# Kernel optimization log

Measured on AMD Instinct MI355X. Metric: run time of the kernel, lower is better.

Reference implementation:

```python
import jax, jax.numpy as jnp
import numpy as np

B = 16384      # batch
D_IN = 512     # layer_channels[0]
D = 1024       # hidden width (layer_channels[1..4])
R = 16         # num_relations
SCALE = 0.02


def setup_inputs() -> dict:
    key = jax.random.key(0)
    ks = jax.random.split(key, 8)
    return {
        "x": jax.random.normal(ks[0], (B, D_IN), dtype=jnp.float32),
        "relations": jax.random.randint(ks[1], (B,), 0, R, dtype=jnp.int32),
        # non-relation dense stack (2 layers)
        "W0": jax.random.normal(ks[2], (D_IN, D), dtype=jnp.float32) * SCALE,
        "b0": jnp.zeros((D,), dtype=jnp.float32),
        "W1": jax.random.normal(ks[3], (D, D), dtype=jnp.float32) * SCALE,
        "b1": jnp.zeros((D,), dtype=jnp.float32),
        # relation-aware layers (3 layers due to the module's range(i, num_layers))
        "RW1": jax.random.normal(ks[4], (R, D, D), dtype=jnp.float32) * SCALE,
        "Rb1": jnp.zeros((R, D), dtype=jnp.float32),
        "RW2": jax.random.normal(ks[5], (R, D, D), dtype=jnp.float32) * SCALE,
        "Rb2": jnp.zeros((R, D), dtype=jnp.float32),
        "RW3": jax.random.normal(ks[6], (R, D, D), dtype=jnp.float32) * SCALE,
        "Rb3": jnp.zeros((R, D), dtype=jnp.float32),
    }


def _relation_linear(h, W, b, relations):
    """Per-sample weight selection: out[n] = h[n] @ W[rel[n]] + b[rel[n]].
    Computed as R masked GEMMs to avoid materializing per-sample [B,D,D] weights.
    """
    out = jnp.zeros((h.shape[0], W.shape[2]), dtype=h.dtype)
    for r in range(W.shape[0]):  # fixed small expert set -> ok to unroll
        mask = (relations == r)[:, None]
        out = out + jnp.where(mask, h @ W[r] + b[r], jnp.zeros((), h.dtype))
    return out


def reference(x, relations, W0, b0, W1, b1, RW1, Rb1, RW2, Rb2, RW3, Rb3):
    # non_relation_pred: Linear -> ReLU -> (dropout=identity), twice
    h = jax.nn.relu(x @ W0 + b0)
    h = jax.nn.relu(h @ W1 + b1)
    # relation layers: relu+dropout between, none after last; bn disabled
    h = jax.nn.relu(_relation_linear(h, RW1, Rb1, relations))
    h = jax.nn.relu(_relation_linear(h, RW2, Rb2, relations))
    h = _relation_linear(h, RW3, Rb3, relations)
    return h
```

## Files before the change

### kernel.cpp

```cpp
#include <hip/hip_runtime.h>
#include <stdint.h>

#define B_ROWS   16384
#define D_IN     512
#define N_DIM    1024
#define NREL     16
#define TM       128
#define TN       128
#define BK       32
#define MAX_TILES 144
#define PADDED_ROWS (MAX_TILES * TM)

typedef __bf16 bf16x8 __attribute__((ext_vector_type(8)));
typedef float  f32x4  __attribute__((ext_vector_type(4)));

__device__ __forceinline__ uint16_t f2bf(float f) {
  union { float f; uint32_t u; } v; v.f = f;
  return (uint16_t)((v.u + 0x7fffu + ((v.u >> 16) & 1u)) >> 16);
}

__device__ __forceinline__ void async_cp16(const uint16_t* g, uint16_t* l) {
  __builtin_amdgcn_global_load_lds(
      (__attribute__((address_space(1))) void*)(g),
      (__attribute__((address_space(3))) void*)(l), 16, 0, 0);
}

__global__ void setup_kernel(const int* __restrict__ rel, int* __restrict__ rowidx,
                             int* __restrict__ texp, int* __restrict__ tval) {
  __shared__ int cnt[NREL], segstart[NREL], cursor[NREL];
  const int t = threadIdx.x;
  const int nt_ = blockDim.x;
  if (t < NREL) { cnt[t] = 0; cursor[t] = 0; }
  __syncthreads();
  for (int i = t; i < B_ROWS; i += nt_) atomicAdd(&cnt[rel[i]], 1);
  __syncthreads();
  if (t == 0) {
    int slot = 0, tile = 0;
    for (int r = 0; r < NREL; r++) {
      segstart[r] = slot;
      const int c = cnt[r];
      const int nt = (c + TM - 1) / TM;
      for (int k = 0; k < nt; k++) {
        texp[tile + k] = r;
        const int rem = c - k * TM;
        tval[tile + k] = rem < TM ? rem : TM;
      }
      tile += nt; slot += nt * TM;
    }
    for (; tile < MAX_TILES; tile++) { texp[tile] = 0; tval[tile] = 0; }
  }
  __syncthreads();
  for (int i = t; i < PADDED_ROWS; i += nt_) rowidx[i] = 0;
  __syncthreads();
  for (int i = t; i < B_ROWS; i += nt_) {
    const int r = rel[i];
    const int p = atomicAdd(&cursor[r], 1);
    rowidx[segstart[r] + p] = i;
  }
}

__global__ void conv_x_kernel(const float* __restrict__ in, uint16_t* __restrict__ out, int n4) {
  const int i = blockIdx.x * blockDim.x + threadIdx.x;
  if (i < n4) {
    const float4 v = ((const float4*)in)[i];
    uint2 o;
    o.x = (uint32_t)f2bf(v.x) | ((uint32_t)f2bf(v.y) << 16);
    o.y = (uint32_t)f2bf(v.z) | ((uint32_t)f2bf(v.w) << 16);
    ((uint2*)out)[i] = o;
  }
}

__global__ __launch_bounds__(256)
void transpose_conv_kernel(const float* __restrict__ W, uint16_t* __restrict__ Wt,
                           int K, int N) {
  __shared__ uint32_t t32[64][33];
  const size_t mat = (size_t)K * N;
  const float*    Wp  = W  + mat * blockIdx.z;
  uint16_t*       Wtp = Wt + mat * blockIdx.z;
  const int n0 = blockIdx.x * 64, k0 = blockIdx.y * 64;
  const int tx = threadIdx.x & 15;
  const int ty = threadIdx.x >> 4;
  #pragma unroll
  for (int rb = 0; rb < 2; rb++) {
    const int kp = rb * 16 + ty;
    const int k  = k0 + kp * 2;
    const float4 r0 = *(const float4*)&Wp[(size_t)k * N + n0 + tx * 4];
    const float4 r1 = *(const float4*)&Wp[(size_t)(k + 1) * N + n0 + tx * 4];
    t32[tx * 4 + 0][kp] = (uint32_t)f2bf(r0.x) | ((uint32_t)f2bf(r1.x) << 16);
    t32[tx * 4 + 1][kp] = (uint32_t)f2bf(r0.y) | ((uint32_t)f2bf(r1.y) << 16);
    t32[tx * 4 + 2][kp] = (uint32_t)f2bf(r0.z) | ((uint32_t)f2bf(r1.z) << 16);
    t32[tx * 4 + 3][kp] = (uint32_t)f2bf(r0.w) | ((uint32_t)f2bf(r1.w) << 16);
  }
  __syncthreads();
  #pragma unroll
  for (int rb = 0; rb < 4; rb++) {
    const int nl = rb * 16 + ty;
    uint2 v; v.x = t32[nl][2 * tx]; v.y = t32[nl][2 * tx + 1];
    *(uint2*)&Wtp[(size_t)(n0 + nl) * K + k0 + tx * 4] = v;
  }
}

template<bool GATHER, bool EXPERT, bool RELU, bool SCATTER>
__global__ __launch_bounds__(256)
void gemm_kernel(const uint16_t* __restrict__ A, const uint16_t* __restrict__ W,
                 const float* __restrict__ bias, void* __restrict__ outp,
                 const int* __restrict__ rowidx, const int* __restrict__ texp,
                 const int* __restrict__ tval, int K) {
  __shared__ uint16_t sA[2][TM * BK];
  __shared__ uint16_t sB[2][TN * BK];

  const int tid = threadIdx.x;
  const int w = tid >> 6, l = tid & 63;

  const int lin = blockIdx.x;
  const int xcd = lin & 7;
  const int j   = lin >> 3;
  const int mpx = gridDim.x >> 6;
  const int my  = xcd * mpx + (j >> 3);
  const int nx  = j & 7;
  const int m0 = my * TM;
  const int n0 = nx * TN;

  int e = 0, valid = TM;
  if (EXPERT) {
    e = texp[my];
    valid = tval[my];
    if (valid == 0) return;
  }

  const int row0   = 16 * w + (l >> 2);
  const int sel    = (row0 ^ (row0 >> 2)) & 3;
  const int koff   = ((l & 3) ^ sel) * 8;
  int ar0 = m0 + row0, ar1 = m0 + 64 + row0;
  if (GATHER) { ar0 = rowidx[ar0]; ar1 = rowidx[ar1]; }
  const uint16_t* srcA0 = A + (size_t)ar0 * K + koff;
  const uint16_t* srcA1 = A + (size_t)ar1 * K + koff;
  const uint16_t* Wb    = W + (size_t)e * N_DIM * K;
  const uint16_t* srcB0 = Wb + (size_t)(n0 + row0) * K + koff;
  const uint16_t* srcB1 = Wb + (size_t)(n0 + 64 + row0) * K + koff;
  uint16_t* ldsA0 = &sA[0][w * 512 + l * 8];
  uint16_t* ldsA1 = &sA[0][2048 + w * 512 + l * 8];
  uint16_t* ldsB0 = &sB[0][w * 512 + l * 8];
  uint16_t* ldsB1 = &sB[0][2048 + w * 512 + l * 8];

  const int wm = w >> 1, wn = w & 1;
  const int q = l >> 4, r16 = l & 15;
  const int selr = (r16 ^ (r16 >> 2)) & 3;
  const int cq = (q ^ selr) * 8;

  f32x4 acc[4][4];
  #pragma unroll
  for (int i = 0; i < 4; i++)
    #pragma unroll
    for (int jj = 0; jj < 4; jj++) {
      f32x4 z = {0.f, 0.f, 0.f, 0.f};
      acc[i][jj] = z;
    }

  const int nIter = K / BK;

  async_cp16(srcA0, ldsA0);
  async_cp16(srcA1, ldsA1);
  async_cp16(srcB0, ldsB0);
  async_cp16(srcB1, ldsB1);

  for (int k = 0; k < nIter; k++) {
    const int cur = k & 1;
    if (k + 1 < nIter) {
      const int koff2 = (k + 1) * BK;
      const int boff  = (cur ^ 1) * 4096;
      async_cp16(srcA0 + koff2, ldsA0 + boff);
      async_cp16(srcA1 + koff2, ldsA1 + boff);
      async_cp16(srcB0 + koff2, ldsB0 + boff);
      async_cp16(srcB1 + koff2, ldsB1 + boff);
      asm volatile("s_waitcnt vmcnt(4)" ::: "memory");
    } else {
      asm volatile("s_waitcnt vmcnt(0)" ::: "memory");
    }
    __builtin_amdgcn_s_barrier();

    bf16x8 af[4], bf[4];
    #pragma unroll
    for (int i = 0; i < 4; i++) {
      af[i] = *(const bf16x8*)(&sA[cur][(wm * 64 + i * 16 + r16) * BK + cq]);
      bf[i] = *(const bf16x8*)(&sB[cur][(wn * 64 + i * 16 + r16) * BK + cq]);
    }
    #pragma unroll
    for (int i = 0; i < 4; i++)
      #pragma unroll
      for (int jj = 0; jj < 4; jj++)
        acc[i][jj] = __builtin_amdgcn_mfma_f32_16x16x32_bf16(af[i], bf[jj], acc[i][jj], 0, 0, 0);

    __builtin_amdgcn_s_barrier();
  }

  float bj[4];
  #pragma unroll
  for (int jj = 0; jj < 4; jj++)
    bj[jj] = bias[(size_t)e * N_DIM + n0 + wn * 64 + jj * 16 + r16];

  #pragma unroll
  for (int i = 0; i < 4; i++) {
    #pragma unroll
    for (int r = 0; r < 4; r++) {
      const int rl = wm * 64 + i * 16 + q * 4 + r;
      if (SCATTER) {
        if (rl < valid) {
          const int orow = rowidx[m0 + rl];
          float* o = (float*)outp + (size_t)orow * N_DIM + n0 + wn * 64 + r16;
          #pragma unroll
          for (int jj = 0; jj < 4; jj++) {
            float v = acc[i][jj][r] + bj[jj];
            if (RELU) v = fmaxf(v, 0.f);
            o[jj * 16] = v;
          }
        }
      } else {
        uint16_t* o = (uint16_t*)outp + (size_t)(m0 + rl) * N_DIM + n0 + wn * 64 + r16;
        #pragma unroll
        for (int jj = 0; jj < 4; jj++) {
          float v = acc[i][jj][r] + bj[jj];
          if (RELU) v = fmaxf(v, 0.f);
          o[jj * 16] = f2bf(v);
        }
      }
    }
  }
}

extern "C" void kernel_launch(void* const* d_in, const int* in_sizes, int n_in,
                              void* d_out, int out_size, void* d_ws, size_t ws_size,
                              hipStream_t stream) {
  const float* x   = (const float*)d_in[0];
  const int*   rel = (const int*)d_in[1];
  const float* W0  = (const float*)d_in[2];
  const float* b0  = (const float*)d_in[3];
  const float* W1  = (const float*)d_in[4];
  const float* b1  = (const float*)d_in[5];
  const float* RW1 = (const float*)d_in[6];
  const float* Rb1 = (const float*)d_in[7];
  const float* RW2 = (const float*)d_in[8];
  const float* Rb2 = (const float*)d_in[9];
  const float* RW3 = (const float*)d_in[10];
  const float* Rb3 = (const float*)d_in[11];
  float* out = (float*)d_out;

  char* ws = (char*)d_ws;
  uint16_t* xb = (uint16_t*)(ws);
  uint16_t* wt = (uint16_t*)(ws + (size_t)(16u << 20));
  uint16_t* ha = (uint16_t*)(ws + (size_t)(48u << 20));
  uint16_t* hb = (uint16_t*)(ws + (size_t)(84u << 20));
  int* rowidx = (int*)(ws + (size_t)(120u << 20));
  int* texp   = rowidx + PADDED_ROWS;
  int* tval   = texp + MAX_TILES;

  const dim3 blk(256);
  const dim3 gDense(8 * (B_ROWS / TM));
  const dim3 gRel(8 * MAX_TILES);

  setup_kernel<<<dim3(1), dim3(1024), 0, stream>>>(rel, rowidx, texp, tval);
  conv_x_kernel<<<dim3((B_ROWS * D_IN) / 4 / 256), blk, 0, stream>>>(x, xb, (B_ROWS * D_IN) / 4);

  transpose_conv_kernel<<<dim3(N_DIM / 64, D_IN / 64, 1), blk, 0, stream>>>(W0, wt, D_IN, N_DIM);
  gemm_kernel<false, false, true, false><<<gDense, blk, 0, stream>>>(
      xb, wt, b0, ha, nullptr, nullptr, nullptr, D_IN);

  transpose_conv_kernel<<<dim3(N_DIM / 64, N_DIM / 64, 1), blk, 0, stream>>>(W1, wt, N_DIM, N_DIM);
  gemm_kernel<false, false, true, false><<<gDense, blk, 0, stream>>>(
      ha, wt, b1, hb, nullptr, nullptr, nullptr, N_DIM);

  transpose_conv_kernel<<<dim3(N_DIM / 64, N_DIM / 64, NREL), blk, 0, stream>>>(RW1, wt, N_DIM, N_DIM);
  gemm_kernel<true, true, true, false><<<gRel, blk, 0, stream>>>(
      hb, wt, Rb1, ha, rowidx, texp, tval, N_DIM);

  transpose_conv_kernel<<<dim3(N_DIM / 64, N_DIM / 64, NREL), blk, 0, stream>>>(RW2, wt, N_DIM, N_DIM);
  gemm_kernel<false, true, true, false><<<gRel, blk, 0, stream>>>(
      ha, wt, Rb2, hb, rowidx, texp, tval, N_DIM);

  transpose_conv_kernel<<<dim3(N_DIM / 64, N_DIM / 64, NREL), blk, 0, stream>>>(RW3, wt, N_DIM, N_DIM);
  gemm_kernel<false, true, false, true><<<gRel, blk, 0, stream>>>(
      hb, wt, Rb3, out, rowidx, texp, tval, N_DIM);

  (void)in_sizes; (void)n_in; (void)out_size; (void)ws_size;
}
```

Baseline: 517.5 us.

## Deepen GEMM LDS pipeline to four stages with fragment prefetch and setprio

Replaces the double-buffered async global-to-LDS loop with a four-stage ring buffer. Four K-slices are kept in flight, and the LDS fragments for the next slice are read into registers while the current MFMAs run. The loop now uses a single barrier per iteration instead of two, and it raises wave priority around the MFMA block. The aim is to hide global-load latency and LDS read latency behind matrix math. In exchange, LDS per block doubles to 64KB, which may lower the number of resident blocks per CU.

```diff
diff --git a/kernel.cpp b/kernel.cpp
--- a/kernel.cpp
+++ b/kernel.cpp
@@ -106,8 +106,8 @@
                  const float* __restrict__ bias, void* __restrict__ outp,
                  const int* __restrict__ rowidx, const int* __restrict__ texp,
                  const int* __restrict__ tval, int K) {
-  __shared__ uint16_t sA[2][TM * BK];
-  __shared__ uint16_t sB[2][TN * BK];
+  __shared__ uint16_t sA[4][TM * BK];
+  __shared__ uint16_t sB[4][TN * BK];
 
   const int tid = threadIdx.x;
   const int w = tid >> 6, l = tid & 63;
@@ -138,10 +138,7 @@
   const uint16_t* Wb    = W + (size_t)e * N_DIM * K;
   const uint16_t* srcB0 = Wb + (size_t)(n0 + row0) * K + koff;
   const uint16_t* srcB1 = Wb + (size_t)(n0 + 64 + row0) * K + koff;
-  uint16_t* ldsA0 = &sA[0][w * 512 + l * 8];
-  uint16_t* ldsA1 = &sA[0][2048 + w * 512 + l * 8];
-  uint16_t* ldsB0 = &sB[0][w * 512 + l * 8];
-  uint16_t* ldsB1 = &sB[0][2048 + w * 512 + l * 8];
+  const int lo = w * 512 + l * 8;
 
   const int wm = w >> 1, wn = w & 1;
   const int q = l >> 4, r16 = l & 15;
@@ -157,42 +154,69 @@
       acc[i][jj] = z;
     }
 
-  const int nIter = K / BK;
-
-  async_cp16(srcA0, ldsA0);
-  async_cp16(srcA1, ldsA1);
-  async_cp16(srcB0, ldsB0);
-  async_cp16(srcB1, ldsB1);
-
-  for (int k = 0; k < nIter; k++) {
-    const int cur = k & 1;
-    if (k + 1 < nIter) {
-      const int koff2 = (k + 1) * BK;
-      const int boff  = (cur ^ 1) * 4096;
-      async_cp16(srcA0 + koff2, ldsA0 + boff);
-      async_cp16(srcA1 + koff2, ldsA1 + boff);
-      async_cp16(srcB0 + koff2, ldsB0 + boff);
-      async_cp16(srcB1 + koff2, ldsB1 + boff);
-      asm volatile("s_waitcnt vmcnt(4)" ::: "memory");
-    } else {
-      asm volatile("s_waitcnt vmcnt(0)" ::: "memory");
-    }
-    __builtin_amdgcn_s_barrier();
-
-    bf16x8 af[4], bf[4];
+  bf16x8 af[4], bf[4];
+
+  auto STAGE = [&](int h) {
+    const int s  = h & 3;
+    const int ko = h * BK;
+    async_cp16(srcA0 + ko, &sA[s][lo]);
+    async_cp16(srcA1 + ko, &sA[s][2048 + lo]);
+    async_cp16(srcB0 + ko, &sB[s][lo]);
+    async_cp16(srcB1 + ko, &sB[s][2048 + lo]);
+  };
+  auto READF = [&](int h) {
+    const int s = h & 3;
     #pragma unroll
     for (int i = 0; i < 4; i++) {
-      af[i] = *(const bf16x8*)(&sA[cur][(wm * 64 + i * 16 + r16) * BK + cq]);
-      bf[i] = *(const bf16x8*)(&sB[cur][(wn * 64 + i * 16 + r16) * BK + cq]);
+      af[i] = *(const bf16x8*)(&sA[s][(wm * 64 + i * 16 + r16) * BK + cq]);
+      bf[i] = *(const bf16x8*)(&sB[s][(wn * 64 + i * 16 + r16) * BK + cq]);
     }
+  };
+  auto MFMAS = [&]() {
     #pragma unroll
     for (int i = 0; i < 4; i++)
       #pragma unroll
       for (int jj = 0; jj < 4; jj++)
         acc[i][jj] = __builtin_amdgcn_mfma_f32_16x16x32_bf16(af[i], bf[jj], acc[i][jj], 0, 0, 0);
-
+  };
+
+  const int NPH = K / BK;
+
+  STAGE(0); STAGE(1); STAGE(2); STAGE(3);
+  asm volatile("s_waitcnt vmcnt(0)" ::: "memory");
+  __builtin_amdgcn_s_barrier();
+  READF(0);
+  asm volatile("s_waitcnt lgkmcnt(0)" ::: "memory");
+
+  for (int p = 0; p <= NPH - 5; ++p) {
     __builtin_amdgcn_s_barrier();
-  }
+    STAGE(p + 4);
+    __builtin_amdgcn_s_setprio(1);
+    MFMAS();
+    __builtin_amdgcn_s_setprio(0);
+    READF(p + 1);
+    asm volatile("s_waitcnt lgkmcnt(0)" ::: "memory");
+    asm volatile("s_waitcnt vmcnt(8)" ::: "memory");
+  }
+
+  __builtin_amdgcn_s_barrier();
+  __builtin_amdgcn_s_setprio(1); MFMAS(); __builtin_amdgcn_s_setprio(0);
+  READF(NPH - 3);
+  asm volatile("s_waitcnt lgkmcnt(0)" ::: "memory");
+  asm volatile("s_waitcnt vmcnt(4)" ::: "memory");
+
+  __builtin_amdgcn_s_barrier();
+  __builtin_amdgcn_s_setprio(1); MFMAS(); __builtin_amdgcn_s_setprio(0);
+  READF(NPH - 2);
+  asm volatile("s_waitcnt lgkmcnt(0)" ::: "memory");
+  asm volatile("s_waitcnt vmcnt(0)" ::: "memory");
+
+  __builtin_amdgcn_s_barrier();
+  __builtin_amdgcn_s_setprio(1); MFMAS(); __builtin_amdgcn_s_setprio(0);
+  READF(NPH - 1);
+  asm volatile("s_waitcnt lgkmcnt(0)" ::: "memory");
+
+  MFMAS();
 
   float bj[4];
   #pragma unroll
```

Result: slower. 556.6 us (+7.6%).

## Enlarge GEMM tiles to 256x256 with deep 8-slot async LDS pipeline

Applied to the files above, without the earlier changes.

Replaces the 128x128, 256-thread GEMM with 256x256 tiles on 512 threads (8 waves, each computing a 128x64 sub-tile). K is loaded in 64-wide chunks through an 8-slot LDS ring filled with async global-to-LDS copies, interleaved with MFMA phases that raise wave priority. Relation layers now gather and scatter rows uniformly through rowidx instead of keeping a compacted layout between layers. The goal is more data reuse per loaded byte and better overlap of loads with MFMA work, at the cost of 128KB LDS per block, more registers, and more padding waste in the per-relation tiles.

```diff
diff --git a/kernel.cpp b/kernel.cpp
--- a/kernel.cpp
+++ b/kernel.cpp
@@ -5,10 +5,8 @@
 #define D_IN     512
 #define N_DIM    1024
 #define NREL     16
-#define TM       128
-#define TN       128
-#define BK       32
-#define MAX_TILES 144
+#define TM       256
+#define MAX_TILES 80
 #define PADDED_ROWS (MAX_TILES * TM)
 
 typedef __bf16 bf16x8 __attribute__((ext_vector_type(8)));
@@ -100,14 +98,26 @@
   }
 }
 
-template<bool GATHER, bool EXPERT, bool RELU, bool SCATTER>
-__global__ __launch_bounds__(256)
+#define MFMA_PAIR(JP)                                                         \
+  _Pragma("unroll")                                                           \
+  for (int i = 0; i < 8; i++) {                                               \
+    acc[i][2*(JP)]   = __builtin_amdgcn_mfma_f32_16x16x32_bf16(af[i], bf[0], acc[i][2*(JP)], 0, 0, 0);   \
+    acc[i][2*(JP)+1] = __builtin_amdgcn_mfma_f32_16x16x32_bf16(af[i], bf[1], acc[i][2*(JP)+1], 0, 0, 0); \
+  }
+#define LDA_FRAGS(SL)                                                         \
+  _Pragma("unroll")                                                           \
+  for (int i = 0; i < 8; i++) af[i] = *(const bf16x8*)&lds[(SL) + abase + i * 512];
+#define LDB_FRAGS(SL, JP)                                                     \
+  bf[0] = *(const bf16x8*)&lds[(SL) + bbase + ((JP) * 2 + 0) * 512];          \
+  bf[1] = *(const bf16x8*)&lds[(SL) + bbase + ((JP) * 2 + 1) * 512];
+
+template<bool REL, bool RELU, bool F32OUT>
+__global__ __launch_bounds__(512, 2)
 void gemm_kernel(const uint16_t* __restrict__ A, const uint16_t* __restrict__ W,
                  const float* __restrict__ bias, void* __restrict__ outp,
                  const int* __restrict__ rowidx, const int* __restrict__ texp,
                  const int* __restrict__ tval, int K) {
-  __shared__ uint16_t sA[2][TM * BK];
-  __shared__ uint16_t sB[2][TN * BK];
+  __shared__ uint16_t lds[8 * 8192];
 
   const int tid = threadIdx.x;
   const int w = tid >> 6, l = tid & 63;
@@ -115,82 +125,111 @@
   const int lin = blockIdx.x;
   const int xcd = lin & 7;
   const int j   = lin >> 3;
-  const int mpx = gridDim.x >> 6;
-  const int my  = xcd * mpx + (j >> 3);
-  const int nx  = j & 7;
+  const int mpx = gridDim.x >> 5;
+  const int my  = xcd * mpx + (j >> 2);
+  const int nx  = j & 3;
   const int m0 = my * TM;
-  const int n0 = nx * TN;
+  const int n0 = nx * TM;
 
   int e = 0, valid = TM;
-  if (EXPERT) {
+  if (REL) {
     e = texp[my];
     valid = tval[my];
     if (valid == 0) return;
   }
 
-  const int row0   = 16 * w + (l >> 2);
-  const int sel    = (row0 ^ (row0 >> 2)) & 3;
-  const int koff   = ((l & 3) ^ sel) * 8;
-  int ar0 = m0 + row0, ar1 = m0 + 64 + row0;
-  if (GATHER) { ar0 = rowidx[ar0]; ar1 = rowidx[ar1]; }
-  const uint16_t* srcA0 = A + (size_t)ar0 * K + koff;
-  const uint16_t* srcA1 = A + (size_t)ar1 * K + koff;
-  const uint16_t* Wb    = W + (size_t)e * N_DIM * K;
-  const uint16_t* srcB0 = Wb + (size_t)(n0 + row0) * K + koff;
-  const uint16_t* srcB1 = Wb + (size_t)(n0 + 64 + row0) * K + koff;
-  uint16_t* ldsA0 = &sA[0][w * 512 + l * 8];
-  uint16_t* ldsA1 = &sA[0][2048 + w * 512 + l * 8];
-  uint16_t* ldsB0 = &sB[0][w * 512 + l * 8];
-  uint16_t* ldsB1 = &sB[0][2048 + w * 512 + l * 8];
-
-  const int wm = w >> 1, wn = w & 1;
-  const int q = l >> 4, r16 = l & 15;
-  const int selr = (r16 ^ (r16 >> 2)) & 3;
-  const int cq = (q ^ selr) * 8;
-
-  f32x4 acc[4][4];
-  #pragma unroll
-  for (int i = 0; i < 4; i++)
+  const int rlo  = l >> 2;
+  const int clog = (l & 3) ^ (rlo & 3);
+  const uint16_t* pA[2]; const uint16_t* pB[2];
+  const uint16_t* We = W + (size_t)e * N_DIM * K;
+  #pragma unroll
+  for (int jj = 0; jj < 2; jj++) {
+    const int b  = 2 * w + jj;
+    const int rr = 16 * b + rlo;
+    int gr = m0 + rr;
+    if (REL) gr = rowidx[gr];
+    pA[jj] = A  + (size_t)gr * K + clog * 8;
+    pB[jj] = We + (size_t)(n0 + rr) * K + clog * 8;
+  }
+
+  const int wm = w >> 2, wn = w & 3;
+  const int q16 = l >> 4, r16 = l & 15;
+  const int phys = q16 ^ (r16 & 3);
+  const int abase = (wm * 128 + r16) * 32 + phys * 8;
+  const int bbase = (wn * 64  + r16) * 32 + phys * 8;
+
+  f32x4 acc[8][4];
+  #pragma unroll
+  for (int i = 0; i < 8; i++)
     #pragma unroll
     for (int jj = 0; jj < 4; jj++) {
       f32x4 z = {0.f, 0.f, 0.f, 0.f};
       acc[i][jj] = z;
     }
-
-  const int nIter = K / BK;
-
-  async_cp16(srcA0, ldsA0);
-  async_cp16(srcA1, ldsA1);
-  async_cp16(srcB0, ldsB0);
-  async_cp16(srcB1, ldsB1);
-
-  for (int k = 0; k < nIter; k++) {
-    const int cur = k & 1;
-    if (k + 1 < nIter) {
-      const int koff2 = (k + 1) * BK;
-      const int boff  = (cur ^ 1) * 4096;
-      async_cp16(srcA0 + koff2, ldsA0 + boff);
-      async_cp16(srcA1 + koff2, ldsA1 + boff);
-      async_cp16(srcB0 + koff2, ldsB0 + boff);
-      async_cp16(srcB1 + koff2, ldsB1 + boff);
-      asm volatile("s_waitcnt vmcnt(4)" ::: "memory");
-    } else {
-      asm volatile("s_waitcnt vmcnt(0)" ::: "memory");
-    }
-    __builtin_amdgcn_s_barrier();
-
-    bf16x8 af[4], bf[4];
-    #pragma unroll
-    for (int i = 0; i < 4; i++) {
-      af[i] = *(const bf16x8*)(&sA[cur][(wm * 64 + i * 16 + r16) * BK + cq]);
-      bf[i] = *(const bf16x8*)(&sB[cur][(wn * 64 + i * 16 + r16) * BK + cq]);
-    }
-    #pragma unroll
-    for (int i = 0; i < 4; i++)
-      #pragma unroll
-      for (int jj = 0; jj < 4; jj++)
-        acc[i][jj] = __builtin_amdgcn_mfma_f32_16x16x32_bf16(af[i], bf[jj], acc[i][jj], 0, 0, 0);
-
+  bf16x8 af[8], bf[2];
+
+  auto STAGE = [&](int h) {
+    const int sl = (h & 7) * 8192;
+    const int c  = h & 3;
+    const int ko = (h >> 2) * 64 + (c >> 1) * 32;
+    const uint16_t* g0 = (c & 1) ? pB[0] : pA[0];
+    const uint16_t* g1 = (c & 1) ? pB[1] : pA[1];
+    async_cp16(g0 + ko, &lds[sl + (2 * w + 0) * 512 + l * 8]);
+    async_cp16(g1 + ko, &lds[sl + (2 * w + 1) * 512 + l * 8]);
+  };
+
+  const int NT = K >> 6;
+
+  #pragma unroll
+  for (int h = 0; h < 6; h++) STAGE(h);
+  asm volatile("s_waitcnt vmcnt(8)" ::: "memory");
+  __builtin_amdgcn_s_barrier();
+
+  for (int T = 0; T < NT; ++T) {
+    const int p0 = 4 * T;
+    const int slA0 = ((p0    ) & 7) * 8192;
+    const int slB0 = ((p0 + 1) & 7) * 8192;
+    const int slA1 = ((p0 + 2) & 7) * 8192;
+    const int slB1 = ((p0 + 3) & 7) * 8192;
+    const bool s01 = (T <= NT - 2);
+    const bool s23 = (T <= NT - 3);
+
+    LDA_FRAGS(slA0);
+    LDB_FRAGS(slB0, 0);
+    if (s01) STAGE(p0 + 6);
+    __builtin_amdgcn_s_barrier();
+    __builtin_amdgcn_s_setprio(1);
+    MFMA_PAIR(0);
+    __builtin_amdgcn_s_setprio(0);
+    __builtin_amdgcn_s_barrier();
+
+    LDB_FRAGS(slB0, 1);
+    if (s01) STAGE(p0 + 7);
+    __builtin_amdgcn_s_barrier();
+    __builtin_amdgcn_s_setprio(1);
+    MFMA_PAIR(1);
+    __builtin_amdgcn_s_setprio(0);
+    if (T < NT - 1) { asm volatile("s_waitcnt vmcnt(8)" ::: "memory"); }
+    else            { asm volatile("s_waitcnt vmcnt(0)" ::: "memory"); }
+    __builtin_amdgcn_s_barrier();
+
+    LDA_FRAGS(slA1);
+    LDB_FRAGS(slB1, 0);
+    if (s23) STAGE(p0 + 8);
+    __builtin_amdgcn_s_barrier();
+    __builtin_amdgcn_s_setprio(1);
+    MFMA_PAIR(0);
+    __builtin_amdgcn_s_setprio(0);
+    __builtin_amdgcn_s_barrier();
+
+    LDB_FRAGS(slB1, 1);
+    if (s23) STAGE(p0 + 9);
+    __builtin_amdgcn_s_barrier();
+    __builtin_amdgcn_s_setprio(1);
+    MFMA_PAIR(1);
+    __builtin_amdgcn_s_setprio(0);
+    if (T < NT - 2)       { asm volatile("s_waitcnt vmcnt(8)" ::: "memory"); }
+    else if (T == NT - 2) { asm volatile("s_waitcnt vmcnt(4)" ::: "memory"); }
     __builtin_amdgcn_s_barrier();
   }
 
@@ -200,23 +239,23 @@
     bj[jj] = bias[(size_t)e * N_DIM + n0 + wn * 64 + jj * 16 + r16];
 
   #pragma unroll
-  for (int i = 0; i < 4; i++) {
+  for (int i = 0; i < 8; i++) {
     #pragma unroll
     for (int r = 0; r < 4; r++) {
-      const int rl = wm * 64 + i * 16 + q * 4 + r;
-      if (SCATTER) {
-        if (rl < valid) {
-          const int orow = rowidx[m0 + rl];
-          float* o = (float*)outp + (size_t)orow * N_DIM + n0 + wn * 64 + r16;
-          #pragma unroll
-          for (int jj = 0; jj < 4; jj++) {
-            float v = acc[i][jj][r] + bj[jj];
-            if (RELU) v = fmaxf(v, 0.f);
-            o[jj * 16] = v;
-          }
+      const int rl = wm * 128 + i * 16 + q16 * 4 + r;
+      if (REL && rl >= valid) continue;
+      int orow = m0 + rl;
+      if (REL) orow = rowidx[m0 + rl];
+      if (F32OUT) {
+        float* o = (float*)outp + (size_t)orow * N_DIM + n0 + wn * 64 + r16;
+        #pragma unroll
+        for (int jj = 0; jj < 4; jj++) {
+          float v = acc[i][jj][r] + bj[jj];
+          if (RELU) v = fmaxf(v, 0.f);
+          o[jj * 16] = v;
         }
       } else {
-        uint16_t* o = (uint16_t*)outp + (size_t)(m0 + rl) * N_DIM + n0 + wn * 64 + r16;
+        uint16_t* o = (uint16_t*)outp + (size_t)orow * N_DIM + n0 + wn * 64 + r16;
         #pragma unroll
         for (int jj = 0; jj < 4; jj++) {
           float v = acc[i][jj][r] + bj[jj];
@@ -248,38 +287,39 @@
   char* ws = (char*)d_ws;
   uint16_t* xb = (uint16_t*)(ws);
   uint16_t* wt = (uint16_t*)(ws + (size_t)(16u << 20));
-  uint16_t* ha = (uint16_t*)(ws + (size_t)(48u << 20));
-  uint16_t* hb = (uint16_t*)(ws + (size_t)(84u << 20));
-  int* rowidx = (int*)(ws + (size_t)(120u << 20));
+  uint16_t* hA = (uint16_t*)(ws + (size_t)(48u << 20));
+  uint16_t* hB = (uint16_t*)(ws + (size_t)(80u << 20));
+  int* rowidx = (int*)(ws + (size_t)(112u << 20));
   int* texp   = rowidx + PADDED_ROWS;
   int* tval   = texp + MAX_TILES;
 
   const dim3 blk(256);
-  const dim3 gDense(8 * (B_ROWS / TM));
-  const dim3 gRel(8 * MAX_TILES);
+  const dim3 gblk(512);
+  const dim3 gDense((B_ROWS / TM) * 4);
+  const dim3 gRel(MAX_TILES * 4);
 
   setup_kernel<<<dim3(1), dim3(1024), 0, stream>>>(rel, rowidx, texp, tval);
   conv_x_kernel<<<dim3((B_ROWS * D_IN) / 4 / 256), blk, 0, stream>>>(x, xb, (B_ROWS * D_IN) / 4);
 
   transpose_conv_kernel<<<dim3(N_DIM / 64, D_IN / 64, 1), blk, 0, stream>>>(W0, wt, D_IN, N_DIM);
-  gemm_kernel<false, false, true, false><<<gDense, blk, 0, stream>>>(
-      xb, wt, b0, ha, nullptr, nullptr, nullptr, D_IN);
+  gemm_kernel<false, true, false><<<gDense, gblk, 0, stream>>>(
+      xb, wt, b0, hA, nullptr, nullptr, nullptr, D_IN);
 
   transpose_conv_kernel<<<dim3(N_DIM / 64, N_DIM / 64, 1), blk, 0, stream>>>(W1, wt, N_DIM, N_DIM);
-  gemm_kernel<false, false, true, false><<<gDense, blk, 0, stream>>>(
-      ha, wt, b1, hb, nullptr, nullptr, nullptr, N_DIM);
+  gemm_kernel<false, true, false><<<gDense, gblk, 0, stream>>>(
+      hA, wt, b1, hB, nullptr, nullptr, nullptr, N_DIM);
 
   transpose_conv_kernel<<<dim3(N_DIM / 64, N_DIM / 64, NREL), blk, 0, stream>>>(RW1, wt, N_DIM, N_DIM);
-  gemm_kernel<true, true, true, false><<<gRel, blk, 0, stream>>>(
-      hb, wt, Rb1, ha, rowidx, texp, tval, N_DIM);
+  gemm_kernel<true, true, false><<<gRel, gblk, 0, stream>>>(
+      hB, wt, Rb1, hA, rowidx, texp, tval, N_DIM);
 
   transpose_conv_kernel<<<dim3(N_DIM / 64, N_DIM / 64, NREL), blk, 0, stream>>>(RW2, wt, N_DIM, N_DIM);
-  gemm_kernel<false, true, true, false><<<gRel, blk, 0, stream>>>(
-      ha, wt, Rb2, hb, rowidx, texp, tval, N_DIM);
+  gemm_kernel<true, true, false><<<gRel, gblk, 0, stream>>>(
+      hA, wt, Rb2, hB, rowidx, texp, tval, N_DIM);
 
   transpose_conv_kernel<<<dim3(N_DIM / 64, N_DIM / 64, NREL), blk, 0, stream>>>(RW3, wt, N_DIM, N_DIM);
-  gemm_kernel<false, true, false, true><<<gRel, blk, 0, stream>>>(
-      hb, wt, Rb3, out, rowidx, texp, tval, N_DIM);
+  gemm_kernel<true, false, true><<<gRel, gblk, 0, stream>>>(
+      hB, wt, Rb3, out, rowidx, texp, tval, N_DIM);
 
   (void)in_sizes; (void)n_in; (void)out_size; (void)ws_size;
 }
```

New measurement: 586.0 us. 13.2% more time.
